# Kernel optimization log

Hardware: AMD Instinct MI355X
Metric: run time of the kernel (lower is better)

## Reference

```python
import jax, jax.numpy as jnp
import numpy as np

B, S, D, H = 4, 2048, 1024, 16
HD = D // H


def setup_inputs() -> dict:
    key = jax.random.key(0)
    ks = jax.random.split(key, 11)
    sc = 0.02
    return {
        "q": jax.random.normal(ks[0], (B, S, D), jnp.float32),
        "k": jax.random.normal(ks[1], (B, S, D), jnp.float32),
        "v": jax.random.normal(ks[2], (B, S, D), jnp.float32),
        "wq_w": jax.random.normal(ks[3], (D, D), jnp.float32) * sc,
        "wq_b": jax.random.normal(ks[4], (D,), jnp.float32) * sc,
        "wk_w": jax.random.normal(ks[5], (D, D), jnp.float32) * sc,
        "wk_b": jax.random.normal(ks[6], (D,), jnp.float32) * sc,
        "wv_w": jax.random.normal(ks[7], (D, D), jnp.float32) * sc,
        "wv_b": jax.random.normal(ks[8], (D,), jnp.float32) * sc,
        "wo_w": jax.random.normal(ks[9], (D, D), jnp.float32) * sc,
        "wo_b": jax.random.normal(ks[10], (D,), jnp.float32) * sc,
    }


def _heads(x):
    # [B,S,D] -> [B,H,S,HD]
    return x.reshape(B, S, H, HD).transpose(0, 2, 1, 3)


def reference(q, k, v, wq_w, wq_b, wk_w, wk_b, wv_w, wv_b, wo_w, wo_b):
    # nn.Linear: y = x @ W^T + b
    Q = _heads(q @ wq_w.T + wq_b)
    K = _heads(k @ wk_w.T + wk_b)
    V = _heads(v @ wv_w.T + wv_b)
    scale = 1.0 / jnp.sqrt(jnp.float32(HD))
    scores = jnp.einsum("bhqd,bhkd->bhqk", Q, K) * scale
    weights = jax.nn.softmax(scores, axis=-1)  # dropout p=0 -> identity
    ctx = jnp.einsum("bhqk,bhkd->bhqd", weights, V)  # [B,H,S,HD]
    merged = ctx.transpose(0, 2, 1, 3).reshape(B, S, D)
    out = merged @ wo_w.T + wo_b
    return out, ctx
```

## Files before the change

kernel.cpp:

```cpp
#include <hip/hip_runtime.h>
#include <hip/hip_bf16.h>

#define HDD 64
#define NH 16
#define SEQ 2048
#define DM 1024
#define BB 4

using bf16x8 = __attribute__((ext_vector_type(8))) short;
using bf16x4 = __attribute__((ext_vector_type(4))) short;
using floatx4 = __attribute__((ext_vector_type(4))) float;
typedef unsigned int u32;

__device__ __forceinline__ short f2bf(float f) {
    __hip_bfloat16 h = __float2bfloat16(f);
    union { __hip_bfloat16 h; short s; } c;
    c.h = h;
    return c.s;
}

__device__ __forceinline__ void stage8f(short* dst, const float* s) {
    float4 a = *(const float4*)s;
    float4 b = *(const float4*)(s + 4);
    bf16x8 r;
    r[0] = f2bf(a.x); r[1] = f2bf(a.y); r[2] = f2bf(a.z); r[3] = f2bf(a.w);
    r[4] = f2bf(b.x); r[5] = f2bf(b.y); r[6] = f2bf(b.z); r[7] = f2bf(b.w);
    *(bf16x8*)dst = r;
}

__global__ __launch_bounds__(256) void wconv_kernel(
    const float* __restrict__ w0, const float* __restrict__ w1,
    const float* __restrict__ w2, const float* __restrict__ w3,
    short* __restrict__ o0, short* __restrict__ o1,
    short* __restrict__ o2, short* __restrict__ o3)
{
    const int z = blockIdx.y;
    const float* src = (z == 0) ? w0 : (z == 1) ? w1 : (z == 2) ? w2 : w3;
    short* dst       = (z == 0) ? o0 : (z == 1) ? o1 : (z == 2) ? o2 : o3;
    size_t i = ((size_t)blockIdx.x * 256 + threadIdx.x) * 8;
    stage8f(dst + i, src + i);
}

__global__ __launch_bounds__(256) void proj_kernel(
    const float* __restrict__ q, const float* __restrict__ k, const float* __restrict__ v,
    const short* __restrict__ wqb, const float* __restrict__ bq,
    const short* __restrict__ wkb, const float* __restrict__ bk,
    const short* __restrict__ wvb, const float* __restrict__ bv,
    short* __restrict__ Qh, short* __restrict__ Kh, short* __restrict__ Vh)
{
    const int z = blockIdx.z;
    const float* X  = (z == 0) ? q   : (z == 1) ? k   : v;
    const short* Wb = (z == 0) ? wqb : (z == 1) ? wkb : wvb;
    const float* Bp = (z == 0) ? bq  : (z == 1) ? bk  : bv;
    short* Dst      = (z == 0) ? Qh  : (z == 1) ? Kh  : Vh;
    const float qscale = (z == 0) ? (0.125f * 1.44269504088896f) : 1.0f;

    const int m0 = blockIdx.x * 128;
    const int n0 = blockIdx.y * 128;
    const int tid = threadIdx.x;
    const int w = tid >> 6, lane = tid & 63, lc = lane & 15, lq = lane >> 4;
    const int wm = w >> 1, wn = w & 1;

    __shared__ alignas(16) short As[128 * 40];
    __shared__ alignas(16) short Bs[128 * 40];

    floatx4 acc[4][4];
#pragma unroll
    for (int i = 0; i < 4; i++)
#pragma unroll
        for (int j = 0; j < 4; j++) acc[i][j] = floatx4{0.f, 0.f, 0.f, 0.f};

    for (int kt = 0; kt < DM / 32; ++kt) {
        __syncthreads();
#pragma unroll
        for (int c = 0; c < 2; ++c) {
            int chunk = c * 256 + tid;
            int row = chunk >> 2;
            int col = (chunk & 3) * 8;
            stage8f(As + row * 40 + col, X + (size_t)(m0 + row) * DM + kt * 32 + col);
            *(bf16x8*)(Bs + row * 40 + col) =
                *(const bf16x8*)(Wb + (size_t)(n0 + row) * DM + kt * 32 + col);
        }
        __syncthreads();

        bf16x8 aF[4], bF[4];
#pragma unroll
        for (int i = 0; i < 4; i++)
            aF[i] = *(const bf16x8*)(As + (wm * 64 + i * 16 + lc) * 40 + lq * 8);
#pragma unroll
        for (int j = 0; j < 4; j++)
            bF[j] = *(const bf16x8*)(Bs + (wn * 64 + j * 16 + lc) * 40 + lq * 8);
        __builtin_amdgcn_s_setprio(1);
#pragma unroll
        for (int i = 0; i < 4; i++)
#pragma unroll
            for (int j = 0; j < 4; j++)
                acc[i][j] = __builtin_amdgcn_mfma_f32_16x16x32_bf16(aF[i], bF[j], acc[i][j], 0, 0, 0);
        __builtin_amdgcn_s_setprio(0);
    }

#pragma unroll
    for (int j = 0; j < 4; j++) {
        int n = n0 + wn * 64 + j * 16 + lc;
        float bias = Bp[n];
        int h = n >> 6, hd = n & 63;
#pragma unroll
        for (int i = 0; i < 4; i++) {
#pragma unroll
            for (int r = 0; r < 4; r++) {
                int m = m0 + wm * 64 + i * 16 + lq * 4 + r;
                int b = m >> 11, s = m & 2047;
                float val = (acc[i][j][r] + bias) * qscale;
                Dst[(((size_t)(b * NH + h)) * SEQ + s) * HDD + hd] = f2bf(val);
            }
        }
    }
}

__global__ __launch_bounds__(512) void attn_kernel(
    const short* __restrict__ Qh, const short* __restrict__ Kh,
    const short* __restrict__ Vh, float* __restrict__ ctxout,
    short* __restrict__ ctxb)
{
    const int linear = blockIdx.y * 16 + blockIdx.x;
    const int swz = (linear & 7) * 128 + (linear >> 3);
    const int qb = swz & 15;
    const int bh = swz >> 4;

    const int tid = threadIdx.x;
    const int w = tid >> 6, lane = tid & 63, lc = lane & 15, lq = lane >> 4;
    const int qbase = qb * 128 + w * 16;

    const short* Qp = Qh + (size_t)bh * SEQ * HDD;
    const short* Kp = Kh + (size_t)bh * SEQ * HDD;
    const short* Vp = Vh + (size_t)bh * SEQ * HDD;

    __shared__ alignas(16) short Vt[2][64 * 72];

    bf16x8 aQ[2];
#pragma unroll
    for (int f = 0; f < 2; ++f)
        aQ[f] = *(const bf16x8*)(Qp + (size_t)(qbase + lc) * HDD + f * 32 + lq * 8);

    float mOld = -1e30f, lSum = 0.f;
    floatx4 accO[4];
#pragma unroll
    for (int dt = 0; dt < 4; dt++) accO[dt] = floatx4{0.f, 0.f, 0.f, 0.f};

    const int kv2 = (tid >> 4) * 2;
    const int d0 = (tid & 15) * 4;
    const int swzb = ((d0 >> 3) & 7) << 3;
    const int kvs_w = kv2 ^ swzb;

    {
        const short* vp = Vp + (size_t)kv2 * HDD + d0;
        bf16x4 v0 = *(const bf16x4*)vp;
        bf16x4 v1 = *(const bf16x4*)(vp + HDD);
#pragma unroll
        for (int i = 0; i < 4; i++) {
            u32 pk = ((u32)(unsigned short)v0[i]) | (((u32)(unsigned short)v1[i]) << 16);
            *(u32*)(&Vt[0][(d0 + i) * 72 + kvs_w]) = pk;
        }
    }
    __syncthreads();

    const int NT = SEQ / 64;
    for (int kt = 0; kt < NT; ++kt) {
        const int cur = kt & 1;
        const int kv0 = kt * 64;

        bf16x4 nv0{}, nv1{};
        const bool have = (kt + 1 < NT);
        if (have) {
            const short* nvp = Vp + (size_t)(kv0 + 64 + kv2) * HDD + d0;
            nv0 = *(const bf16x4*)nvp;
            nv1 = *(const bf16x4*)(nvp + HDD);
        }

        floatx4 sc[4];
        __builtin_amdgcn_s_setprio(1);
#pragma unroll
        for (int nt = 0; nt < 4; nt++) {
            floatx4 sv = floatx4{0.f, 0.f, 0.f, 0.f};
#pragma unroll
            for (int f = 0; f < 2; f++) {
                bf16x8 bK = *(const bf16x8*)(Kp + (size_t)(kv0 + nt * 16 + lc) * HDD + f * 32 + lq * 8);
                sv = __builtin_amdgcn_mfma_f32_16x16x32_bf16(bK, aQ[f], sv, 0, 0, 0);
            }
            sc[nt] = sv;
        }
        __builtin_amdgcn_s_setprio(0);

        float mx = sc[0][0];
#pragma unroll
        for (int nt = 0; nt < 4; nt++)
#pragma unroll
            for (int r = 0; r < 4; r++) mx = fmaxf(mx, sc[nt][r]);
        mx = fmaxf(mx, __shfl_xor(mx, 16, 64));
        mx = fmaxf(mx, __shfl_xor(mx, 32, 64));
        if (!__all(mx - mOld <= 8.0f)) {
            const float mNew = fmaxf(mOld, mx);
            const float alpha = __builtin_amdgcn_exp2f(mOld - mNew);
            lSum *= alpha;
#pragma unroll
            for (int dt = 0; dt < 4; dt++)
#pragma unroll
                for (int r = 0; r < 4; r++) accO[dt][r] *= alpha;
            mOld = mNew;
        }
        float rsum = 0.f;
#pragma unroll
        for (int nt = 0; nt < 4; nt++)
#pragma unroll
            for (int r = 0; r < 4; r++) {
                float p = __builtin_amdgcn_exp2f(sc[nt][r] - mOld);
                sc[nt][r] = p;
                rsum += p;
            }
        rsum += __shfl_xor(rsum, 16, 64);
        rsum += __shfl_xor(rsum, 32, 64);
        lSum += rsum;

        u32 pw[4][2];
#pragma unroll
        for (int nt = 0; nt < 4; nt++) {
            pw[nt][0] = ((u32)(unsigned short)f2bf(sc[nt][0])) |
                        (((u32)(unsigned short)f2bf(sc[nt][1])) << 16);
            pw[nt][1] = ((u32)(unsigned short)f2bf(sc[nt][2])) |
                        (((u32)(unsigned short)f2bf(sc[nt][3])) << 16);
        }
        const int srcA = ((lq & 1) << 5) + lc;
        const int srcB = srcA + 16;
        const bool selHi = (lq >> 1) != 0;

#pragma unroll
        for (int f = 0; f < 2; f++) {
            u32 a0 = (u32)__shfl((int)pw[2 * f][0], srcA, 64);
            u32 a1 = (u32)__shfl((int)pw[2 * f][1], srcA, 64);
            u32 a2 = (u32)__shfl((int)pw[2 * f][0], srcB, 64);
            u32 a3 = (u32)__shfl((int)pw[2 * f][1], srcB, 64);
            u32 b0 = (u32)__shfl((int)pw[2 * f + 1][0], srcA, 64);
            u32 b1 = (u32)__shfl((int)pw[2 * f + 1][1], srcA, 64);
            u32 b2 = (u32)__shfl((int)pw[2 * f + 1][0], srcB, 64);
            u32 b3 = (u32)__shfl((int)pw[2 * f + 1][1], srcB, 64);
            union { u32 u[4]; bf16x8 v; } P;
            P.u[0] = selHi ? b0 : a0;
            P.u[1] = selHi ? b1 : a1;
            P.u[2] = selHi ? b2 : a2;
            P.u[3] = selHi ? b3 : a3;
            __builtin_amdgcn_s_setprio(1);
#pragma unroll
            for (int dt = 0; dt < 4; dt++) {
                const int d = dt * 16 + lc;
                const int kvs = (f * 32 + lq * 8) ^ (((d >> 3) & 7) << 3);
                bf16x8 bV = *(const bf16x8*)(&Vt[cur][d * 72 + kvs]);
                accO[dt] = __builtin_amdgcn_mfma_f32_16x16x32_bf16(bV, P.v, accO[dt], 0, 0, 0);
            }
            __builtin_amdgcn_s_setprio(0);
        }

        if (have) {
            short* dstb = &Vt[cur ^ 1][0];
#pragma unroll
            for (int i = 0; i < 4; i++) {
                u32 pk = ((u32)(unsigned short)nv0[i]) | (((u32)(unsigned short)nv1[i]) << 16);
                *(u32*)(dstb + (d0 + i) * 72 + kvs_w) = pk;
            }
        }
        __syncthreads();
    }

    const float inv = 1.0f / lSum;
    const size_t rowoff = ((size_t)bh * SEQ + qbase + lc) * HDD;
    float* orow = ctxout + rowoff;
    short* brow = ctxb + rowoff;
#pragma unroll
    for (int dt = 0; dt < 4; dt++) {
        float4 st;
        st.x = accO[dt][0] * inv;
        st.y = accO[dt][1] * inv;
        st.z = accO[dt][2] * inv;
        st.w = accO[dt][3] * inv;
        *(float4*)(orow + dt * 16 + lq * 4) = st;
        uint2 bb;
        bb.x = ((u32)(unsigned short)f2bf(st.x)) | (((u32)(unsigned short)f2bf(st.y)) << 16);
        bb.y = ((u32)(unsigned short)f2bf(st.z)) | (((u32)(unsigned short)f2bf(st.w)) << 16);
        *(uint2*)(brow + dt * 16 + lq * 4) = bb;
    }
}

__global__ __launch_bounds__(256) void outproj_kernel(
    const short* __restrict__ ctxb, const short* __restrict__ wob,
    const float* __restrict__ bo, float* __restrict__ out)
{
    const int m0 = blockIdx.x * 128;
    const int n0 = blockIdx.y * 128;
    const int tid = threadIdx.x;
    const int w = tid >> 6, lane = tid & 63, lc = lane & 15, lq = lane >> 4;
    const int wm = w >> 1, wn = w & 1;

    __shared__ alignas(16) short As[128 * 40];
    __shared__ alignas(16) short Bs[128 * 40];

    floatx4 acc[4][4];
#pragma unroll
    for (int i = 0; i < 4; i++)
#pragma unroll
        for (int j = 0; j < 4; j++) acc[i][j] = floatx4{0.f, 0.f, 0.f, 0.f};

    for (int kt = 0; kt < DM / 32; ++kt) {
        __syncthreads();
#pragma unroll
        for (int c = 0; c < 2; ++c) {
            int chunk = c * 256 + tid;
            int row = chunk >> 2;
            int col = (chunk & 3) * 8;
            int m = m0 + row;
            int b = m >> 11, s = m & 2047;
            int kcol = kt * 32 + col;
            int h = kcol >> 6, hd = kcol & 63;
            *(bf16x8*)(As + row * 40 + col) =
                *(const bf16x8*)(ctxb + (((size_t)(b * NH + h)) * SEQ + s) * HDD + hd);
            *(bf16x8*)(Bs + row * 40 + col) =
                *(const bf16x8*)(wob + (size_t)(n0 + row) * DM + kt * 32 + col);
        }
        __syncthreads();

        bf16x8 aF[4], bF[4];
#pragma unroll
        for (int i = 0; i < 4; i++)
            aF[i] = *(const bf16x8*)(As + (wm * 64 + i * 16 + lc) * 40 + lq * 8);
#pragma unroll
        for (int j = 0; j < 4; j++)
            bF[j] = *(const bf16x8*)(Bs + (wn * 64 + j * 16 + lc) * 40 + lq * 8);
        __builtin_amdgcn_s_setprio(1);
#pragma unroll
        for (int i = 0; i < 4; i++)
#pragma unroll
            for (int j = 0; j < 4; j++)
                acc[i][j] = __builtin_amdgcn_mfma_f32_16x16x32_bf16(aF[i], bF[j], acc[i][j], 0, 0, 0);
        __builtin_amdgcn_s_setprio(0);
    }

#pragma unroll
    for (int j = 0; j < 4; j++) {
        int n = n0 + wn * 64 + j * 16 + lc;
        float bias = bo[n];
#pragma unroll
        for (int i = 0; i < 4; i++) {
#pragma unroll
            for (int r = 0; r < 4; r++) {
                int m = m0 + wm * 64 + i * 16 + lq * 4 + r;
                out[(size_t)m * DM + n] = acc[i][j][r] + bias;
            }
        }
    }
}

extern "C" void kernel_launch(void* const* d_in, const int* in_sizes, int n_in,
                              void* d_out, int out_size, void* d_ws, size_t ws_size,
                              hipStream_t stream) {
    const float* q  = (const float*)d_in[0];
    const float* k  = (const float*)d_in[1];
    const float* v  = (const float*)d_in[2];
    const float* wq = (const float*)d_in[3];
    const float* bq = (const float*)d_in[4];
    const float* wk = (const float*)d_in[5];
    const float* bk = (const float*)d_in[6];
    const float* wv = (const float*)d_in[7];
    const float* bv = (const float*)d_in[8];
    const float* wo = (const float*)d_in[9];
    const float* bo = (const float*)d_in[10];

    float* out0 = (float*)d_out;
    float* ctx  = out0 + (size_t)BB * SEQ * DM;

    const size_t NELEM = (size_t)BB * NH * SEQ * HDD;
    short* Qh   = (short*)d_ws;
    short* Kh   = Qh + NELEM;
    short* Vh   = Kh + NELEM;
    short* ctxb = Vh + NELEM;
    short* Wqb  = ctxb + NELEM;
    short* Wkb  = Wqb + (size_t)DM * DM;
    short* Wvb  = Wkb + (size_t)DM * DM;
    short* Wob  = Wvb + (size_t)DM * DM;

    wconv_kernel<<<dim3(512, 4), 256, 0, stream>>>(wq, wk, wv, wo, Wqb, Wkb, Wvb, Wob);
    proj_kernel<<<dim3(64, 8, 3), 256, 0, stream>>>(q, k, v, Wqb, bq, Wkb, bk, Wvb, bv, Qh, Kh, Vh);
    attn_kernel<<<dim3(16, 64), 512, 0, stream>>>(Qh, Kh, Vh, ctx, ctxb);
    outproj_kernel<<<dim3(64, 8), 256, 0, stream>>>(ctxb, Wob, bo, out0);
}
```

Measured before the change: 561.0 us.

## Pre-convert activations to bf16 and process 128 keys per attention iteration

```diff
diff --git a/kernel.cpp b/kernel.cpp
--- a/kernel.cpp
+++ b/kernel.cpp
@@ -28,28 +28,46 @@
     *(bf16x8*)dst = r;
 }
 
-__global__ __launch_bounds__(256) void wconv_kernel(
+__device__ __forceinline__ float vmax4(floatx4 v) {
+    return fmaxf(fmaxf(v[0], v[1]), fmaxf(v[2], v[3]));
+}
+
+__global__ __launch_bounds__(256) void conv_kernel(
     const float* __restrict__ w0, const float* __restrict__ w1,
     const float* __restrict__ w2, const float* __restrict__ w3,
-    short* __restrict__ o0, short* __restrict__ o1,
-    short* __restrict__ o2, short* __restrict__ o3)
+    const float* __restrict__ x0, const float* __restrict__ x1,
+    const float* __restrict__ x2,
+    short* __restrict__ ow0, short* __restrict__ ow1,
+    short* __restrict__ ow2, short* __restrict__ ow3,
+    short* __restrict__ ox0, short* __restrict__ ox1,
+    short* __restrict__ ox2)
 {
     const int z = blockIdx.y;
-    const float* src = (z == 0) ? w0 : (z == 1) ? w1 : (z == 2) ? w2 : w3;
-    short* dst       = (z == 0) ? o0 : (z == 1) ? o1 : (z == 2) ? o2 : o3;
+    const float* src;
+    short* dst;
+    switch (z) {
+        case 0: src = w0; dst = ow0; break;
+        case 1: src = w1; dst = ow1; break;
+        case 2: src = w2; dst = ow2; break;
+        case 3: src = w3; dst = ow3; break;
+        case 4: src = x0; dst = ox0; break;
+        case 5: src = x1; dst = ox1; break;
+        default: src = x2; dst = ox2; break;
+    }
+    if (z < 4 && blockIdx.x >= 512) return;
     size_t i = ((size_t)blockIdx.x * 256 + threadIdx.x) * 8;
     stage8f(dst + i, src + i);
 }
 
 __global__ __launch_bounds__(256) void proj_kernel(
-    const float* __restrict__ q, const float* __restrict__ k, const float* __restrict__ v,
+    const short* __restrict__ xq, const short* __restrict__ xk, const short* __restrict__ xv,
     const short* __restrict__ wqb, const float* __restrict__ bq,
     const short* __restrict__ wkb, const float* __restrict__ bk,
     const short* __restrict__ wvb, const float* __restrict__ bv,
     short* __restrict__ Qh, short* __restrict__ Kh, short* __restrict__ Vh)
 {
     const int z = blockIdx.z;
-    const float* X  = (z == 0) ? q   : (z == 1) ? k   : v;
+    const short* X  = (z == 0) ? xq  : (z == 1) ? xk  : xv;
     const short* Wb = (z == 0) ? wqb : (z == 1) ? wkb : wvb;
     const float* Bp = (z == 0) ? bq  : (z == 1) ? bk  : bv;
     short* Dst      = (z == 0) ? Qh  : (z == 1) ? Kh  : Vh;
@@ -77,7 +95,8 @@
             int chunk = c * 256 + tid;
             int row = chunk >> 2;
             int col = (chunk & 3) * 8;
-            stage8f(As + row * 40 + col, X + (size_t)(m0 + row) * DM + kt * 32 + col);
+            *(bf16x8*)(As + row * 40 + col) =
+                *(const bf16x8*)(X + (size_t)(m0 + row) * DM + kt * 32 + col);
             *(bf16x8*)(Bs + row * 40 + col) =
                 *(const bf16x8*)(Wb + (size_t)(n0 + row) * DM + kt * 32 + col);
         }
@@ -135,7 +154,7 @@
     const short* Kp = Kh + (size_t)bh * SEQ * HDD;
     const short* Vp = Vh + (size_t)bh * SEQ * HDD;
 
-    __shared__ alignas(16) short Vt[2][64 * 72];
+    __shared__ alignas(16) short Vt[2][2][64 * 72];
 
     bf16x8 aQ[2];
 #pragma unroll
@@ -147,37 +166,44 @@
 #pragma unroll
     for (int dt = 0; dt < 4; dt++) accO[dt] = floatx4{0.f, 0.f, 0.f, 0.f};
 
-    const int kv2 = (tid >> 4) * 2;
-    const int d0 = (tid & 15) * 4;
-    const int swzb = ((d0 >> 3) & 7) << 3;
+    const int half = tid >> 8;
+    const int t8 = tid & 255;
+    const int kv2 = (t8 >> 3) * 2;
+    const int d0 = (t8 & 7) * 8;
+    const int swzb = (t8 & 7) << 3;
     const int kvs_w = kv2 ^ swzb;
 
     {
-        const short* vp = Vp + (size_t)kv2 * HDD + d0;
-        bf16x4 v0 = *(const bf16x4*)vp;
-        bf16x4 v1 = *(const bf16x4*)(vp + HDD);
-#pragma unroll
-        for (int i = 0; i < 4; i++) {
+        const short* vp = Vp + (size_t)(half * 64 + kv2) * HDD + d0;
+        bf16x8 v0 = *(const bf16x8*)vp;
+        bf16x8 v1 = *(const bf16x8*)(vp + HDD);
+        short* dstb = &Vt[0][half][0];
+#pragma unroll
+        for (int i = 0; i < 8; i++) {
             u32 pk = ((u32)(unsigned short)v0[i]) | (((u32)(unsigned short)v1[i]) << 16);
-            *(u32*)(&Vt[0][(d0 + i) * 72 + kvs_w]) = pk;
+            *(u32*)(dstb + (d0 + i) * 72 + kvs_w) = pk;
         }
     }
     __syncthreads();
 
-    const int NT = SEQ / 64;
-    for (int kt = 0; kt < NT; ++kt) {
-        const int cur = kt & 1;
-        const int kv0 = kt * 64;
-
-        bf16x4 nv0{}, nv1{};
-        const bool have = (kt + 1 < NT);
+    const int srcA = ((lq & 1) << 5) + lc;
+    const int srcB = srcA + 16;
+    const bool selHi = (lq >> 1) != 0;
+
+    const int NP = SEQ / 128;
+    for (int kp = 0; kp < NP; ++kp) {
+        const int cur = kp & 1;
+        const int kv0 = kp * 128;
+        const bool have = (kp + 1 < NP);
+
+        bf16x8 nv0{}, nv1{};
         if (have) {
-            const short* nvp = Vp + (size_t)(kv0 + 64 + kv2) * HDD + d0;
-            nv0 = *(const bf16x4*)nvp;
-            nv1 = *(const bf16x4*)(nvp + HDD);
-        }
-
-        floatx4 sc[4];
+            const short* nvp = Vp + (size_t)(kv0 + 128 + half * 64 + kv2) * HDD + d0;
+            nv0 = *(const bf16x8*)nvp;
+            nv1 = *(const bf16x8*)(nvp + HDD);
+        }
+
+        floatx4 sc0[4], sc1[4];
         __builtin_amdgcn_s_setprio(1);
 #pragma unroll
         for (int nt = 0; nt < 4; nt++) {
@@ -187,15 +213,25 @@
                 bf16x8 bK = *(const bf16x8*)(Kp + (size_t)(kv0 + nt * 16 + lc) * HDD + f * 32 + lq * 8);
                 sv = __builtin_amdgcn_mfma_f32_16x16x32_bf16(bK, aQ[f], sv, 0, 0, 0);
             }
-            sc[nt] = sv;
+            sc0[nt] = sv;
+        }
+#pragma unroll
+        for (int nt = 0; nt < 4; nt++) {
+            floatx4 sv = floatx4{0.f, 0.f, 0.f, 0.f};
+#pragma unroll
+            for (int f = 0; f < 2; f++) {
+                bf16x8 bK = *(const bf16x8*)(Kp + (size_t)(kv0 + 64 + nt * 16 + lc) * HDD + f * 32 + lq * 8);
+                sv = __builtin_amdgcn_mfma_f32_16x16x32_bf16(bK, aQ[f], sv, 0, 0, 0);
+            }
+            sc1[nt] = sv;
         }
         __builtin_amdgcn_s_setprio(0);
 
-        float mx = sc[0][0];
-#pragma unroll
-        for (int nt = 0; nt < 4; nt++)
-#pragma unroll
-            for (int r = 0; r < 4; r++) mx = fmaxf(mx, sc[nt][r]);
+        float ma = fmaxf(fmaxf(vmax4(sc0[0]), vmax4(sc0[1])),
+                         fmaxf(vmax4(sc0[2]), vmax4(sc0[3])));
+        float mb = fmaxf(fmaxf(vmax4(sc1[0]), vmax4(sc1[1])),
+                         fmaxf(vmax4(sc1[2]), vmax4(sc1[3])));
+        float mx = fmaxf(ma, mb);
         mx = fmaxf(mx, __shfl_xor(mx, 16, 64));
         mx = fmaxf(mx, __shfl_xor(mx, 32, 64));
         if (!__all(mx - mOld <= 8.0f)) {
@@ -208,61 +244,69 @@
                 for (int r = 0; r < 4; r++) accO[dt][r] *= alpha;
             mOld = mNew;
         }
-        float rsum = 0.f;
-#pragma unroll
-        for (int nt = 0; nt < 4; nt++)
+
+        float part[8];
+#pragma unroll
+        for (int nt = 0; nt < 4; nt++) {
+            floatx4 p0 = sc0[nt], p1 = sc1[nt];
 #pragma unroll
             for (int r = 0; r < 4; r++) {
-                float p = __builtin_amdgcn_exp2f(sc[nt][r] - mOld);
-                sc[nt][r] = p;
-                rsum += p;
-            }
+                p0[r] = __builtin_amdgcn_exp2f(p0[r] - mOld);
+                p1[r] = __builtin_amdgcn_exp2f(p1[r] - mOld);
+            }
+            sc0[nt] = p0; sc1[nt] = p1;
+            part[nt]     = (p0[0] + p0[1]) + (p0[2] + p0[3]);
+            part[4 + nt] = (p1[0] + p1[1]) + (p1[2] + p1[3]);
+        }
+        float rsum = ((part[0] + part[1]) + (part[2] + part[3])) +
+                     ((part[4] + part[5]) + (part[6] + part[7]));
         rsum += __shfl_xor(rsum, 16, 64);
         rsum += __shfl_xor(rsum, 32, 64);
         lSum += rsum;
 
-        u32 pw[4][2];
-#pragma unroll
-        for (int nt = 0; nt < 4; nt++) {
-            pw[nt][0] = ((u32)(unsigned short)f2bf(sc[nt][0])) |
-                        (((u32)(unsigned short)f2bf(sc[nt][1])) << 16);
-            pw[nt][1] = ((u32)(unsigned short)f2bf(sc[nt][2])) |
-                        (((u32)(unsigned short)f2bf(sc[nt][3])) << 16);
-        }
-        const int srcA = ((lq & 1) << 5) + lc;
-        const int srcB = srcA + 16;
-        const bool selHi = (lq >> 1) != 0;
-
-#pragma unroll
-        for (int f = 0; f < 2; f++) {
-            u32 a0 = (u32)__shfl((int)pw[2 * f][0], srcA, 64);
-            u32 a1 = (u32)__shfl((int)pw[2 * f][1], srcA, 64);
-            u32 a2 = (u32)__shfl((int)pw[2 * f][0], srcB, 64);
-            u32 a3 = (u32)__shfl((int)pw[2 * f][1], srcB, 64);
-            u32 b0 = (u32)__shfl((int)pw[2 * f + 1][0], srcA, 64);
-            u32 b1 = (u32)__shfl((int)pw[2 * f + 1][1], srcA, 64);
-            u32 b2 = (u32)__shfl((int)pw[2 * f + 1][0], srcB, 64);
-            u32 b3 = (u32)__shfl((int)pw[2 * f + 1][1], srcB, 64);
-            union { u32 u[4]; bf16x8 v; } P;
-            P.u[0] = selHi ? b0 : a0;
-            P.u[1] = selHi ? b1 : a1;
-            P.u[2] = selHi ? b2 : a2;
-            P.u[3] = selHi ? b3 : a3;
-            __builtin_amdgcn_s_setprio(1);
-#pragma unroll
-            for (int dt = 0; dt < 4; dt++) {
-                const int d = dt * 16 + lc;
-                const int kvs = (f * 32 + lq * 8) ^ (((d >> 3) & 7) << 3);
-                bf16x8 bV = *(const bf16x8*)(&Vt[cur][d * 72 + kvs]);
-                accO[dt] = __builtin_amdgcn_mfma_f32_16x16x32_bf16(bV, P.v, accO[dt], 0, 0, 0);
-            }
-            __builtin_amdgcn_s_setprio(0);
+#pragma unroll
+        for (int t = 0; t < 2; t++) {
+            floatx4* sc = (t == 0) ? sc0 : sc1;
+            const short* vtb = &Vt[cur][t][0];
+            u32 pw[4][2];
+#pragma unroll
+            for (int nt = 0; nt < 4; nt++) {
+                pw[nt][0] = ((u32)(unsigned short)f2bf(sc[nt][0])) |
+                            (((u32)(unsigned short)f2bf(sc[nt][1])) << 16);
+                pw[nt][1] = ((u32)(unsigned short)f2bf(sc[nt][2])) |
+                            (((u32)(unsigned short)f2bf(sc[nt][3])) << 16);
+            }
+#pragma unroll
+            for (int f = 0; f < 2; f++) {
+                u32 a0 = (u32)__shfl((int)pw[2 * f][0], srcA, 64);
+                u32 a1 = (u32)__shfl((int)pw[2 * f][1], srcA, 64);
+                u32 a2 = (u32)__shfl((int)pw[2 * f][0], srcB, 64);
+                u32 a3 = (u32)__shfl((int)pw[2 * f][1], srcB, 64);
+                u32 b0 = (u32)__shfl((int)pw[2 * f + 1][0], srcA, 64);
+                u32 b1 = (u32)__shfl((int)pw[2 * f + 1][1], srcA, 64);
+                u32 b2 = (u32)__shfl((int)pw[2 * f + 1][0], srcB, 64);
+                u32 b3 = (u32)__shfl((int)pw[2 * f + 1][1], srcB, 64);
+                union { u32 u[4]; bf16x8 v; } P;
+                P.u[0] = selHi ? b0 : a0;
+                P.u[1] = selHi ? b1 : a1;
+                P.u[2] = selHi ? b2 : a2;
+                P.u[3] = selHi ? b3 : a3;
+                __builtin_amdgcn_s_setprio(1);
+#pragma unroll
+                for (int dt = 0; dt < 4; dt++) {
+                    const int d = dt * 16 + lc;
+                    const int kvs = (f * 32 + lq * 8) ^ (((d >> 3) & 7) << 3);
+                    bf16x8 bV = *(const bf16x8*)(vtb + d * 72 + kvs);
+                    accO[dt] = __builtin_amdgcn_mfma_f32_16x16x32_bf16(bV, P.v, accO[dt], 0, 0, 0);
+                }
+                __builtin_amdgcn_s_setprio(0);
+            }
         }
 
         if (have) {
-            short* dstb = &Vt[cur ^ 1][0];
-#pragma unroll
-            for (int i = 0; i < 4; i++) {
+            short* dstb = &Vt[cur ^ 1][half][0];
+#pragma unroll
+            for (int i = 0; i < 8; i++) {
                 u32 pk = ((u32)(unsigned short)nv0[i]) | (((u32)(unsigned short)nv1[i]) << 16);
                 *(u32*)(dstb + (d0 + i) * 72 + kvs_w) = pk;
             }
@@ -384,9 +428,14 @@
     short* Wkb  = Wqb + (size_t)DM * DM;
     short* Wvb  = Wkb + (size_t)DM * DM;
     short* Wob  = Wvb + (size_t)DM * DM;
-
-    wconv_kernel<<<dim3(512, 4), 256, 0, stream>>>(wq, wk, wv, wo, Wqb, Wkb, Wvb, Wob);
-    proj_kernel<<<dim3(64, 8, 3), 256, 0, stream>>>(q, k, v, Wqb, bq, Wkb, bk, Wvb, bv, Qh, Kh, Vh);
+    short* Xq = (short*)out0;
+    short* Xk = Xq + NELEM;
+    short* Xv = ctxb;
+
+    conv_kernel<<<dim3(4096, 7), 256, 0, stream>>>(
+        wq, wk, wv, wo, q, k, v, Wqb, Wkb, Wvb, Wob, Xq, Xk, Xv);
+    proj_kernel<<<dim3(64, 8, 3), 256, 0, stream>>>(
+        Xq, Xk, Xv, Wqb, bq, Wkb, bk, Wvb, bv, Qh, Kh, Vh);
     attn_kernel<<<dim3(16, 64), 512, 0, stream>>>(Qh, Kh, Vh, ctx, ctxb);
     outproj_kernel<<<dim3(64, 8), 256, 0, stream>>>(ctxb, Wob, bo, out0);
 }
```

Result: faster. 516.0 us (-8.0%).
